# Performance work log

Hardware: AMD Instinct MI355X
Metric: run time of the kernel (lower is better)

Reference implementation:

```python
import jax, jax.numpy as jnp
import numpy as np

B, T, D, H = 4, 2048, 1024, 16
HD = D // H  # head_dim = 64


def _make_freqs():
    # standard RoPE angles: theta_i = 10000^{-2i/hd}
    inv_freq = 1.0 / (10000.0 ** (np.arange(0, HD, 2, dtype=np.float32) / HD))  # [HD/2]
    angles = np.arange(T, dtype=np.float32)[:, None] * inv_freq[None, :]        # [T, HD/2]
    return jnp.asarray(np.cos(angles)), jnp.asarray(np.sin(angles))


def setup_inputs() -> dict:
    key = jax.random.key(0)
    ks = jax.random.split(key, 5)
    freqs_cos, freqs_sin = _make_freqs()
    s = 1.0 / np.sqrt(D)
    return {
        "q": jax.random.normal(ks[0], (B, T, D), jnp.float32),
        "freqs_cos": freqs_cos,
        "freqs_sin": freqs_sin,
        "qkv_w": jax.random.normal(ks[1], (3 * D, D), jnp.float32) * s,
        "qkv_b": jax.random.normal(ks[2], (3 * D,), jnp.float32) * 0.01,
        "o_w": jax.random.normal(ks[3], (D, D), jnp.float32) * s,
        "o_b": jax.random.normal(ks[4], (D,), jnp.float32) * 0.01,
    }


def _apply_rope(x, cos, sin):
    # x: [B, T, H, HD]; cos/sin: [T, HD/2]
    xr = x.reshape(*x.shape[:-1], HD // 2, 2)
    x0, x1 = xr[..., 0], xr[..., 1]
    c = cos[None, :, None, :]
    s = sin[None, :, None, :]
    o0 = x0 * c - x1 * s
    o1 = x0 * s + x1 * c
    return jnp.stack([o0, o1], axis=-1).reshape(x.shape)


def reference(q, freqs_cos, freqs_sin, qkv_w, qkv_b, o_w, o_b):
    # fused QKV projection (torch Linear: x @ W.T + b)
    qkv = q @ qkv_w.T + qkv_b                      # [B, T, 3D]
    qh, kh, vh = jnp.split(qkv, 3, axis=-1)
    qh = qh.reshape(B, T, H, HD)
    kh = kh.reshape(B, T, H, HD)
    vh = vh.reshape(B, T, H, HD)
    qh = _apply_rope(qh, freqs_cos, freqs_sin)
    kh = _apply_rope(kh, freqs_cos, freqs_sin)
    # scaled dot-product attention, no mask, no dropout (eval)
    scale = 1.0 / np.sqrt(HD)
    scores = jnp.einsum('bqhd,bkhd->bhqk', qh, kh) * scale
    probs = jax.nn.softmax(scores, axis=-1)
    out = jnp.einsum('bhqk,bkhd->bqhd', probs, vh).reshape(B, T, D)
    return out @ o_w.T + o_b
```

## Files before the change

kernel.cpp:

```cpp
#include <hip/hip_runtime.h>

#define B_  4
#define T_  2048
#define D_  1024
#define H_  16
#define HD_ 64
#define M_  8192
#define N1_ 3072
#define K_  1024

typedef __bf16 bf16x8 __attribute__((ext_vector_type(8)));
typedef float  f32x4  __attribute__((ext_vector_type(4)));
typedef float  f32x16 __attribute__((ext_vector_type(16)));

__device__ __forceinline__ unsigned short f2bf(float f) {
  union { float f; unsigned u; } v; v.f = f;
  unsigned u = v.u;
  unsigned r = (u + 0x7fffu + ((u >> 16) & 1u)) >> 16;
  return (unsigned short)r;
}
__device__ __forceinline__ float bf2f(unsigned short h) {
  union { unsigned u; float f; } v; v.u = ((unsigned)h) << 16;
  return v.f;
}
__device__ __forceinline__ unsigned pk2(float a, float b) {
  union { __bf16 h[2]; unsigned u; } t;
  t.h[0] = (__bf16)a; t.h[1] = (__bf16)b;
  return t.u;
}
__device__ __forceinline__ void plswap(unsigned &a, unsigned &b) {
  asm("v_permlane32_swap_b32 %0, %1" : "+v"(a), "+v"(b));
}
__device__ __forceinline__ float fexp2(float x) {
  float r;
  asm("v_exp_f32 %0, %1" : "=v"(r) : "v"(x));
  return r;
}

__device__ __forceinline__ void gl_lds16(const unsigned short* g, unsigned short* l) {
  __builtin_amdgcn_global_load_lds(
      (const __attribute__((address_space(1))) unsigned int*)g,
      (__attribute__((address_space(3))) unsigned int*)l,
      16, 0, 0);
}

#define NQ4  ((M_*K_)/4)
#define NW14 ((N1_*K_)/4)
#define NW24 ((D_*K_)/4)
__global__ void cvt_all(const float* __restrict__ q, const float* __restrict__ w1,
                        const float* __restrict__ w2,
                        unsigned short* __restrict__ qo, unsigned short* __restrict__ w1o,
                        unsigned short* __restrict__ w2o) {
  int i = blockIdx.x * 256 + threadIdx.x;
  const float* in; unsigned short* out; int idx;
  if (i < NQ4)              { in = q;  out = qo;  idx = i; }
  else if (i < NQ4 + NW14)  { in = w1; out = w1o; idx = i - NQ4; }
  else if (i < NQ4 + NW14 + NW24) { in = w2; out = w2o; idx = i - NQ4 - NW14; }
  else return;
  float4 f = ((const float4*)in)[idx];
  ushort4 o;
  o.x = f2bf(f.x); o.y = f2bf(f.y); o.z = f2bf(f.z); o.w = f2bf(f.w);
  ((ushort4*)out)[idx] = o;
}

__global__ __launch_bounds__(256) void gemm_qkv(
    const unsigned short* __restrict__ A,
    const unsigned short* __restrict__ W,
    const float* __restrict__ bias,
    unsigned short* __restrict__ Qg,
    unsigned short* __restrict__ Kg,
    unsigned short* __restrict__ Vt,
    const float* __restrict__ cosb, const float* __restrict__ sinb)
{
  __shared__ unsigned short As[128*64];
  __shared__ unsigned short Bs[128*64];
  const int tid = threadIdx.x;
  const int lane = tid & 63, wave = tid >> 6;
  const int wr = wave >> 1, wc = wave & 1;
  const int lr = lane & 15, lg = lane >> 4;
  const int sw = lr & 7;
  const long m0 = (long)blockIdx.x * 128;
  const int  n0 = blockIdx.y * 128;

  f32x4 acc[4][4];
#pragma unroll
  for (int i = 0; i < 4; ++i)
#pragma unroll
    for (int j = 0; j < 4; ++j) acc[i][j] = (f32x4){0.f,0.f,0.f,0.f};

  for (int kt = 0; kt < K_/64; ++kt) {
    __syncthreads();
#pragma unroll
    for (int p = 0; p < 4; ++p) {
      int slot = p*256 + tid;
      int row = slot >> 3, sc = slot & 7, ch = sc ^ (row & 7);
      gl_lds16(A + (m0 + row)*K_ + kt*64 + ch*8, &As[slot*8]);
      gl_lds16(W + ((long)n0 + row)*K_ + kt*64 + ch*8, &Bs[slot*8]);
    }
    __syncthreads();
#pragma unroll
    for (int kk = 0; kk < 2; ++kk) {
      bf16x8 af[4], bfr[4];
#pragma unroll
      for (int i = 0; i < 4; ++i) {
        af[i]  = *(const bf16x8*)&As[(wr*64 + i*16 + lr)*64 + (((lg + 4*kk) ^ sw) * 8)];
        bfr[i] = *(const bf16x8*)&Bs[(wc*64 + i*16 + lr)*64 + (((lg + 4*kk) ^ sw) * 8)];
      }
#pragma unroll
      for (int i = 0; i < 4; ++i)
#pragma unroll
        for (int j = 0; j < 4; ++j)
          acc[i][j] = __builtin_amdgcn_mfma_f32_16x16x32_bf16(af[i], bfr[j], acc[i][j], 0, 0, 0);
    }
  }

#pragma unroll
  for (int j = 0; j < 4; ++j) {
    int n = n0 + wc*64 + j*16 + lr;
    float bv = bias[n];
    int part = n >> 10;
    int d = n & 1023;
    int h = d >> 6, hd = d & 63;
    if (part == 2) {
#pragma unroll
      for (int i = 0; i < 4; ++i) {
        long m = m0 + wr*64 + i*16 + lg*4;
        int b = (int)(m >> 11), t = (int)(m & 2047);
        ushort4 st;
        st.x = f2bf(acc[i][j][0] + bv);
        st.y = f2bf(acc[i][j][1] + bv);
        st.z = f2bf(acc[i][j][2] + bv);
        st.w = f2bf(acc[i][j][3] + bv);
        *(ushort4*)(Vt + ((long)((b*H_ + h)*HD_ + hd))*T_ + t) = st;
      }
    } else if (part == 0) {
#pragma unroll
      for (int i = 0; i < 4; ++i) {
#pragma unroll
        for (int r = 0; r < 4; ++r) {
          long m = m0 + wr*64 + i*16 + lg*4 + r;
          int b = (int)(m >> 11), t = (int)(m & 2047);
          Qg[(((long)(b*H_ + h))*T_ + t)*HD_ + hd] = f2bf(acc[i][j][r] + bv);
        }
      }
    } else {
      const int u   = hd >> 1;
      const int odd = lr & 1;
#pragma unroll
      for (int i = 0; i < 4; ++i) {
#pragma unroll
        for (int r = 0; r < 4; ++r) {
          long m = m0 + wr*64 + i*16 + lg*4 + r;
          int b = (int)(m >> 11), t = (int)(m & 2047);
          float v = acc[i][j][r] + bv;
          float p = __shfl_xor(v, 1);
          float cu = cosb[t*32 + u], su = sinb[t*32 + u];
          float res = odd ? (p*su + v*cu) : (v*cu - p*su);
          Kg[(((long)(b*H_ + h))*T_ + t)*HD_ + hd] = f2bf(res);
        }
      }
    }
  }
}

__global__ __launch_bounds__(256) void flash_attn(
    const unsigned short* __restrict__ Qg, const unsigned short* __restrict__ Kg,
    const unsigned short* __restrict__ Vt, unsigned short* __restrict__ attn,
    const float* __restrict__ cosb, const float* __restrict__ sinb)
{
  __shared__ unsigned short Ks0[64*64], Vs0[64*64];
  __shared__ unsigned short Ks1[64*64], Vs1[64*64];
  const int tid = threadIdx.x, lane = tid & 63, wave = tid >> 6;
  const int lq = lane & 31, hi = lane >> 5;
  const int id = blockIdx.x;
  const int bh = (id & 7)*8 + ((id >> 3) & 7);
  const int q0 = (id >> 6)*128 + wave*32;
  const long kvbase = (long)bh * T_ * HD_;
  const int fsw = (lq & 7) ^ (lq >> 3);

  bf16x8 qf[4];
  {
    const int tq = q0 + lq;
    const unsigned short* qrow = Qg + kvbase + (long)tq*HD_;
    const float* crow = cosb + tq*32;
    const float* srow = sinb + tq*32;
    const float scl = 0.125f * 1.44269504f;
#pragma unroll
    for (int c = 0; c < 4; ++c) {
      bf16x8 raw = *(const bf16x8*)(qrow + c*16 + hi*8);
      const unsigned short* e = (const unsigned short*)&raw;
      bf16x8 outv;
#pragma unroll
      for (int j = 0; j < 4; ++j) {
        float x0 = bf2f(e[2*j]), x1 = bf2f(e[2*j+1]);
        float cv = crow[c*8 + hi*4 + j], sv = srow[c*8 + hi*4 + j];
        outv[2*j]   = (__bf16)((x0*cv - x1*sv) * scl);
        outv[2*j+1] = (__bf16)((x0*sv + x1*cv) * scl);
      }
      qf[c] = outv;
    }
  }

  bf16x8 onesv;
#pragma unroll
  for (int r = 0; r < 8; ++r) onesv[r] = (__bf16)1.0f;

  f32x16 oA, oB;
  f32x16 lacc;
#pragma unroll
  for (int r = 0; r < 16; ++r) { oA[r] = 0.f; oB[r] = 0.f; lacc[r] = 0.f; }

  const int slotA = tid, slotB = 256 + tid;
  const int rwA = slotA >> 3, rwB = slotB >> 3;
  const int chA = (slotA & 7) ^ ((rwA & 7) ^ ((rwA >> 3) & 7));
  const int chB = (slotB & 7) ^ ((rwB & 7) ^ ((rwB >> 3) & 7));
  const unsigned short* KsrcA = Kg + kvbase + (long)rwA*HD_ + chA*8;
  const unsigned short* KsrcB = Kg + kvbase + (long)rwB*HD_ + chB*8;
  const unsigned short* VsrcA = Vt + (long)(bh*HD_ + rwA)*T_ + chA*8;
  const unsigned short* VsrcB = Vt + (long)(bh*HD_ + rwB)*T_ + chB*8;

#define STAGE0(kt) {                                      \
    gl_lds16(KsrcA + (kt)*64*HD_, &Ks0[slotA*8]);         \
    gl_lds16(KsrcB + (kt)*64*HD_, &Ks0[slotB*8]);         \
    gl_lds16(VsrcA + (kt)*64,     &Vs0[slotA*8]);         \
    gl_lds16(VsrcB + (kt)*64,     &Vs0[slotB*8]);         \
  }
#define STAGE1(kt) {                                      \
    gl_lds16(KsrcA + (kt)*64*HD_, &Ks1[slotA*8]);         \
    gl_lds16(KsrcB + (kt)*64*HD_, &Ks1[slotB*8]);         \
    gl_lds16(VsrcA + (kt)*64,     &Vs1[slotA*8]);         \
    gl_lds16(VsrcB + (kt)*64,     &Vs1[slotB*8]);         \
  }

#define FBODY(KSB, VSB)                                                                   \
  _Pragma("unroll")                                                                       \
  for (int kf = 0; kf < 2; ++kf) {                                                        \
    bf16x8 ka[4];                                                                         \
    _Pragma("unroll")                                                                     \
    for (int c = 0; c < 4; ++c)                                                           \
      ka[c] = *(const bf16x8*)&KSB[(kf*32 + lq)*64 + (((2*c + hi) ^ fsw ^ (kf*4)) * 8)];  \
    f32x16 cf;                                                                            \
    _Pragma("unroll")                                                                     \
    for (int r = 0; r < 16; ++r) cf[r] = 0.f;                                             \
    __builtin_amdgcn_s_setprio(1);                                                        \
    cf = __builtin_amdgcn_mfma_f32_32x32x16_bf16(ka[0], qf[0], cf, 0, 0, 0);              \
    cf = __builtin_amdgcn_mfma_f32_32x32x16_bf16(ka[1], qf[1], cf, 0, 0, 0);              \
    cf = __builtin_amdgcn_mfma_f32_32x32x16_bf16(ka[2], qf[2], cf, 0, 0, 0);              \
    cf = __builtin_amdgcn_mfma_f32_32x32x16_bf16(ka[3], qf[3], cf, 0, 0, 0);              \
    __builtin_amdgcn_s_setprio(0);                                                        \
    float p[16];                                                                          \
    _Pragma("unroll")                                                                     \
    for (int r = 0; r < 16; ++r) p[r] = fexp2(cf[r]);                                     \
    unsigned qx0 = pk2(p[0],  p[1]),  qy0 = pk2(p[2],  p[3]);                             \
    unsigned qx1 = pk2(p[4],  p[5]),  qy1 = pk2(p[6],  p[7]);                             \
    unsigned qx2 = pk2(p[8],  p[9]),  qy2 = pk2(p[10], p[11]);                            \
    unsigned qx3 = pk2(p[12], p[13]), qy3 = pk2(p[14], p[15]);                            \
    plswap(qx0, qx1); plswap(qy0, qy1);                                                   \
    plswap(qx2, qx3); plswap(qy2, qy3);                                                   \
    union { unsigned w[4]; bf16x8 v; } u0, u1;                                            \
    u0.w[0] = qx0; u0.w[1] = qy0; u0.w[2] = qx1; u0.w[3] = qy1;                           \
    u1.w[0] = qx2; u1.w[1] = qy2; u1.w[2] = qx3; u1.w[3] = qy3;                           \
    bf16x8 pf0 = u0.v, pf1 = u1.v;                                                        \
    bf16x8 va00 = *(const bf16x8*)&VSB[(lq)*64      + (((4*kf + 0 + hi) ^ fsw) * 8)];     \
    bf16x8 va01 = *(const bf16x8*)&VSB[(lq)*64      + (((4*kf + 2 + hi) ^ fsw) * 8)];     \
    bf16x8 va10 = *(const bf16x8*)&VSB[(32 + lq)*64 + (((4*kf + 0 + hi) ^ fsw ^ 4) * 8)]; \
    bf16x8 va11 = *(const bf16x8*)&VSB[(32 + lq)*64 + (((4*kf + 2 + hi) ^ fsw ^ 4) * 8)]; \
    __builtin_amdgcn_s_setprio(1);                                                        \
    oA = __builtin_amdgcn_mfma_f32_32x32x16_bf16(va00, pf0, oA, 0, 0, 0);                 \
    oA = __builtin_amdgcn_mfma_f32_32x32x16_bf16(va01, pf1, oA, 0, 0, 0);                 \
    oB = __builtin_amdgcn_mfma_f32_32x32x16_bf16(va10, pf0, oB, 0, 0, 0);                 \
    oB = __builtin_amdgcn_mfma_f32_32x32x16_bf16(va11, pf1, oB, 0, 0, 0);                 \
    lacc = __builtin_amdgcn_mfma_f32_32x32x16_bf16(onesv, pf0, lacc, 0, 0, 0);            \
    lacc = __builtin_amdgcn_mfma_f32_32x32x16_bf16(onesv, pf1, lacc, 0, 0, 0);            \
    __builtin_amdgcn_s_setprio(0);                                                        \
  }

  STAGE0(0);
  __syncthreads();

  for (int kt = 0; kt < T_/64; kt += 2) {
    STAGE1(kt + 1);
    FBODY(Ks0, Vs0);
    __syncthreads();
    if (kt + 2 < T_/64) STAGE0(kt + 2);
    FBODY(Ks1, Vs1);
    __syncthreads();
  }
#undef STAGE0
#undef STAGE1
#undef FBODY

  float l = lacc[0];
  int b = bh >> 4, h = bh & 15;
  float inv = 1.0f / l;
  long rowb = ((long)(b*T_ + q0 + lq))*D_ + h*HD_;
#pragma unroll
  for (int g = 0; g < 4; ++g) {
    ushort4 st;
    st.x = f2bf(oA[4*g+0] * inv);
    st.y = f2bf(oA[4*g+1] * inv);
    st.z = f2bf(oA[4*g+2] * inv);
    st.w = f2bf(oA[4*g+3] * inv);
    *(ushort4*)(attn + rowb + 8*g + 4*hi) = st;
  }
#pragma unroll
  for (int g = 0; g < 4; ++g) {
    ushort4 st;
    st.x = f2bf(oB[4*g+0] * inv);
    st.y = f2bf(oB[4*g+1] * inv);
    st.z = f2bf(oB[4*g+2] * inv);
    st.w = f2bf(oB[4*g+3] * inv);
    *(ushort4*)(attn + rowb + 32 + 8*g + 4*hi) = st;
  }
}

__global__ __launch_bounds__(256) void gemm_out(
    const unsigned short* __restrict__ A,
    const unsigned short* __restrict__ W,
    const float* __restrict__ bias,
    float* __restrict__ C)
{
  __shared__ unsigned short As[128*64];
  __shared__ unsigned short Bs[128*64];
  const int tid = threadIdx.x;
  const int lane = tid & 63, wave = tid >> 6;
  const int wr = wave >> 1, wc = wave & 1;
  const int lr = lane & 15, lg = lane >> 4;
  const int sw = lr & 7;
  const long m0 = (long)blockIdx.x * 128;
  const int  n0 = blockIdx.y * 128;

  f32x4 acc[4][4];
#pragma unroll
  for (int i = 0; i < 4; ++i)
#pragma unroll
    for (int j = 0; j < 4; ++j) acc[i][j] = (f32x4){0.f,0.f,0.f,0.f};

  for (int kt = 0; kt < K_/64; ++kt) {
    __syncthreads();
#pragma unroll
    for (int p = 0; p < 4; ++p) {
      int slot = p*256 + tid;
      int row = slot >> 3, sc = slot & 7, ch = sc ^ (row & 7);
      gl_lds16(A + (m0 + row)*K_ + kt*64 + ch*8, &As[slot*8]);
      gl_lds16(W + ((long)n0 + row)*K_ + kt*64 + ch*8, &Bs[slot*8]);
    }
    __syncthreads();
#pragma unroll
    for (int kk = 0; kk < 2; ++kk) {
      bf16x8 af[4], bfr[4];
#pragma unroll
      for (int i = 0; i < 4; ++i) {
        af[i]  = *(const bf16x8*)&As[(wr*64 + i*16 + lr)*64 + (((lg + 4*kk) ^ sw) * 8)];
        bfr[i] = *(const bf16x8*)&Bs[(wc*64 + i*16 + lr)*64 + (((lg + 4*kk) ^ sw) * 8)];
      }
#pragma unroll
      for (int i = 0; i < 4; ++i)
#pragma unroll
        for (int j = 0; j < 4; ++j)
          acc[i][j] = __builtin_amdgcn_mfma_f32_16x16x32_bf16(af[i], bfr[j], acc[i][j], 0, 0, 0);
    }
  }

#pragma unroll
  for (int j = 0; j < 4; ++j) {
    int n = n0 + wc*64 + j*16 + lr;
    float bv = bias[n];
#pragma unroll
    for (int i = 0; i < 4; ++i) {
#pragma unroll
      for (int r = 0; r < 4; ++r) {
        long m = m0 + wr*64 + i*16 + lg*4 + r;
        C[m*D_ + n] = acc[i][j][r] + bv;
      }
    }
  }
}

extern "C" void kernel_launch(void* const* d_in, const int* in_sizes, int n_in,
                              void* d_out, int out_size, void* d_ws, size_t ws_size,
                              hipStream_t stream)
{
  const float* q     = (const float*)d_in[0];
  const float* fcos  = (const float*)d_in[1];
  const float* fsin  = (const float*)d_in[2];
  const float* qkv_w = (const float*)d_in[3];
  const float* qkv_b = (const float*)d_in[4];
  const float* o_w   = (const float*)d_in[5];
  const float* o_b   = (const float*)d_in[6];
  float* out = (float*)d_out;

  char* ws = (char*)d_ws;
  unsigned short* qbf  = (unsigned short*)(ws);
  unsigned short* w1bf = (unsigned short*)(ws + 16777216);
  unsigned short* w2bf = (unsigned short*)(ws + 16777216 + 6291456);
  unsigned short* Qg   = (unsigned short*)(ws + 25165824);
  unsigned short* Kg   = (unsigned short*)(ws + 41943040);
  unsigned short* Vt   = (unsigned short*)(ws + 58720256);

  int ncvt = NQ4 + NW14 + NW24;
  cvt_all<<<(ncvt + 255)/256, 256, 0, stream>>>(q, qkv_w, o_w, qbf, w1bf, w2bf);

  dim3 g1(M_/128, N1_/128);
  gemm_qkv<<<g1, 256, 0, stream>>>(qbf, w1bf, qkv_b, Qg, Kg, Vt, fcos, fsin);

  unsigned short* attn = qbf;
  flash_attn<<<1024, 256, 0, stream>>>(Qg, Kg, Vt, attn, fcos, fsin);

  dim3 g2(M_/128, D_/128);
  gemm_out<<<g2, 256, 0, stream>>>(attn, w2bf, o_b, out);
}
```

Baseline: 206.5 us.

## Process two query tiles per wave in flash attention, sum row totals with VALU

Each wave now handles two 32-row query tiles, rows q0 and q0+128, and shares every K and V fragment loaded from LDS between them. That doubles the MFMA work per LDS read and halves the grid to 512 blocks. The row-sum MFMAs against a ones vector are replaced by scalar float adds of the exp values plus a cross-half shuffle. The kernel keeps the fixed no-max softmax shape, and the change raises register pressure and may lower occupancy and wave-level parallelism.

```diff
diff --git a/kernel.cpp b/kernel.cpp
--- a/kernel.cpp
+++ b/kernel.cpp
@@ -174,41 +174,41 @@
   const int lq = lane & 31, hi = lane >> 5;
   const int id = blockIdx.x;
   const int bh = (id & 7)*8 + ((id >> 3) & 7);
-  const int q0 = (id >> 6)*128 + wave*32;
+  const int q0 = (id >> 6)*256 + wave*32;
   const long kvbase = (long)bh * T_ * HD_;
   const int fsw = (lq & 7) ^ (lq >> 3);
 
-  bf16x8 qf[4];
+  bf16x8 qfA[4], qfB[4];
   {
-    const int tq = q0 + lq;
-    const unsigned short* qrow = Qg + kvbase + (long)tq*HD_;
-    const float* crow = cosb + tq*32;
-    const float* srow = sinb + tq*32;
     const float scl = 0.125f * 1.44269504f;
 #pragma unroll
-    for (int c = 0; c < 4; ++c) {
-      bf16x8 raw = *(const bf16x8*)(qrow + c*16 + hi*8);
-      const unsigned short* e = (const unsigned short*)&raw;
-      bf16x8 outv;
-#pragma unroll
-      for (int j = 0; j < 4; ++j) {
-        float x0 = bf2f(e[2*j]), x1 = bf2f(e[2*j+1]);
-        float cv = crow[c*8 + hi*4 + j], sv = srow[c*8 + hi*4 + j];
-        outv[2*j]   = (__bf16)((x0*cv - x1*sv) * scl);
-        outv[2*j+1] = (__bf16)((x0*sv + x1*cv) * scl);
-      }
-      qf[c] = outv;
-    }
-  }
-
-  bf16x8 onesv;
-#pragma unroll
-  for (int r = 0; r < 8; ++r) onesv[r] = (__bf16)1.0f;
+    for (int g = 0; g < 2; ++g) {
+      const int tq = q0 + g*128 + lq;
+      const unsigned short* qrow = Qg + kvbase + (long)tq*HD_;
+      const float* crow = cosb + tq*32;
+      const float* srow = sinb + tq*32;
+#pragma unroll
+      for (int c = 0; c < 4; ++c) {
+        bf16x8 raw = *(const bf16x8*)(qrow + c*16 + hi*8);
+        const unsigned short* e = (const unsigned short*)&raw;
+        bf16x8 outv;
+#pragma unroll
+        for (int j = 0; j < 4; ++j) {
+          float x0 = bf2f(e[2*j]), x1 = bf2f(e[2*j+1]);
+          float cv = crow[c*8 + hi*4 + j], sv = srow[c*8 + hi*4 + j];
+          outv[2*j]   = (__bf16)((x0*cv - x1*sv) * scl);
+          outv[2*j+1] = (__bf16)((x0*sv + x1*cv) * scl);
+        }
+        if (g == 0) qfA[c] = outv; else qfB[c] = outv;
+      }
+    }
+  }
 
   f32x16 oA, oB;
-  f32x16 lacc;
-#pragma unroll
-  for (int r = 0; r < 16; ++r) { oA[r] = 0.f; oB[r] = 0.f; lacc[r] = 0.f; }
+  f32x16 oC, oD;
+#pragma unroll
+  for (int r = 0; r < 16; ++r) { oA[r] = 0.f; oB[r] = 0.f; oC[r] = 0.f; oD[r] = 0.f; }
+  float lA = 0.f, lB = 0.f;
 
   const int slotA = tid, slotB = 256 + tid;
   const int rwA = slotA >> 3, rwB = slotB >> 3;
@@ -239,39 +239,65 @@
     _Pragma("unroll")                                                                     \
     for (int c = 0; c < 4; ++c)                                                           \
       ka[c] = *(const bf16x8*)&KSB[(kf*32 + lq)*64 + (((2*c + hi) ^ fsw ^ (kf*4)) * 8)];  \
-    f32x16 cf;                                                                            \
+    f32x16 cfA, cfB;                                                                      \
     _Pragma("unroll")                                                                     \
-    for (int r = 0; r < 16; ++r) cf[r] = 0.f;                                             \
+    for (int r = 0; r < 16; ++r) { cfA[r] = 0.f; cfB[r] = 0.f; }                          \
     __builtin_amdgcn_s_setprio(1);                                                        \
-    cf = __builtin_amdgcn_mfma_f32_32x32x16_bf16(ka[0], qf[0], cf, 0, 0, 0);              \
-    cf = __builtin_amdgcn_mfma_f32_32x32x16_bf16(ka[1], qf[1], cf, 0, 0, 0);              \
-    cf = __builtin_amdgcn_mfma_f32_32x32x16_bf16(ka[2], qf[2], cf, 0, 0, 0);              \
-    cf = __builtin_amdgcn_mfma_f32_32x32x16_bf16(ka[3], qf[3], cf, 0, 0, 0);              \
+    cfA = __builtin_amdgcn_mfma_f32_32x32x16_bf16(ka[0], qfA[0], cfA, 0, 0, 0);           \
+    cfB = __builtin_amdgcn_mfma_f32_32x32x16_bf16(ka[0], qfB[0], cfB, 0, 0, 0);           \
+    cfA = __builtin_amdgcn_mfma_f32_32x32x16_bf16(ka[1], qfA[1], cfA, 0, 0, 0);           \
+    cfB = __builtin_amdgcn_mfma_f32_32x32x16_bf16(ka[1], qfB[1], cfB, 0, 0, 0);           \
+    cfA = __builtin_amdgcn_mfma_f32_32x32x16_bf16(ka[2], qfA[2], cfA, 0, 0, 0);           \
+    cfB = __builtin_amdgcn_mfma_f32_32x32x16_bf16(ka[2], qfB[2], cfB, 0, 0, 0);           \
+    cfA = __builtin_amdgcn_mfma_f32_32x32x16_bf16(ka[3], qfA[3], cfA, 0, 0, 0);           \
+    cfB = __builtin_amdgcn_mfma_f32_32x32x16_bf16(ka[3], qfB[3], cfB, 0, 0, 0);           \
     __builtin_amdgcn_s_setprio(0);                                                        \
-    float p[16];                                                                          \
+    float p[16], p2[16];                                                                  \
     _Pragma("unroll")                                                                     \
-    for (int r = 0; r < 16; ++r) p[r] = fexp2(cf[r]);                                     \
-    unsigned qx0 = pk2(p[0],  p[1]),  qy0 = pk2(p[2],  p[3]);                             \
-    unsigned qx1 = pk2(p[4],  p[5]),  qy1 = pk2(p[6],  p[7]);                             \
-    unsigned qx2 = pk2(p[8],  p[9]),  qy2 = pk2(p[10], p[11]);                            \
-    unsigned qx3 = pk2(p[12], p[13]), qy3 = pk2(p[14], p[15]);                            \
-    plswap(qx0, qx1); plswap(qy0, qy1);                                                   \
-    plswap(qx2, qx3); plswap(qy2, qy3);                                                   \
-    union { unsigned w[4]; bf16x8 v; } u0, u1;                                            \
-    u0.w[0] = qx0; u0.w[1] = qy0; u0.w[2] = qx1; u0.w[3] = qy1;                           \
-    u1.w[0] = qx2; u1.w[1] = qy2; u1.w[2] = qx3; u1.w[3] = qy3;                           \
-    bf16x8 pf0 = u0.v, pf1 = u1.v;                                                        \
+    for (int r = 0; r < 16; ++r) { p[r] = fexp2(cfA[r]); p2[r] = fexp2(cfB[r]); }         \
+    {                                                                                     \
+      float a0 = (p[0]+p[1]) + (p[2]+p[3]);                                               \
+      float a1 = (p[4]+p[5]) + (p[6]+p[7]);                                               \
+      float a2 = (p[8]+p[9]) + (p[10]+p[11]);                                             \
+      float a3 = (p[12]+p[13]) + (p[14]+p[15]);                                           \
+      lA += (a0 + a1) + (a2 + a3);                                                        \
+      float b0 = (p2[0]+p2[1]) + (p2[2]+p2[3]);                                           \
+      float b1 = (p2[4]+p2[5]) + (p2[6]+p2[7]);                                           \
+      float b2 = (p2[8]+p2[9]) + (p2[10]+p2[11]);                                         \
+      float b3 = (p2[12]+p2[13]) + (p2[14]+p2[15]);                                       \
+      lB += (b0 + b1) + (b2 + b3);                                                        \
+    }                                                                                     \
+    unsigned ax0 = pk2(p[0],  p[1]),  ay0 = pk2(p[2],  p[3]);                             \
+    unsigned ax1 = pk2(p[4],  p[5]),  ay1 = pk2(p[6],  p[7]);                             \
+    unsigned ax2 = pk2(p[8],  p[9]),  ay2 = pk2(p[10], p[11]);                            \
+    unsigned ax3 = pk2(p[12], p[13]), ay3 = pk2(p[14], p[15]);                            \
+    plswap(ax0, ax1); plswap(ay0, ay1);                                                   \
+    plswap(ax2, ax3); plswap(ay2, ay3);                                                   \
+    unsigned bx0 = pk2(p2[0],  p2[1]),  by0 = pk2(p2[2],  p2[3]);                         \
+    unsigned bx1 = pk2(p2[4],  p2[5]),  by1 = pk2(p2[6],  p2[7]);                         \
+    unsigned bx2 = pk2(p2[8],  p2[9]),  by2 = pk2(p2[10], p2[11]);                        \
+    unsigned bx3 = pk2(p2[12], p2[13]), by3 = pk2(p2[14], p2[15]);                        \
+    plswap(bx0, bx1); plswap(by0, by1);                                                   \
+    plswap(bx2, bx3); plswap(by2, by3);                                                   \
+    union { unsigned w[4]; bf16x8 v; } uA0, uA1, uB0, uB1;                                \
+    uA0.w[0] = ax0; uA0.w[1] = ay0; uA0.w[2] = ax1; uA0.w[3] = ay1;                       \
+    uA1.w[0] = ax2; uA1.w[1] = ay2; uA1.w[2] = ax3; uA1.w[3] = ay3;                       \
+    uB0.w[0] = bx0; uB0.w[1] = by0; uB0.w[2] = bx1; uB0.w[3] = by1;                       \
+    uB1.w[0] = bx2; uB1.w[1] = by2; uB1.w[2] = bx3; uB1.w[3] = by3;                       \
+    bf16x8 pfA0 = uA0.v, pfA1 = uA1.v, pfB0 = uB0.v, pfB1 = uB1.v;                        \
     bf16x8 va00 = *(const bf16x8*)&VSB[(lq)*64      + (((4*kf + 0 + hi) ^ fsw) * 8)];     \
     bf16x8 va01 = *(const bf16x8*)&VSB[(lq)*64      + (((4*kf + 2 + hi) ^ fsw) * 8)];     \
     bf16x8 va10 = *(const bf16x8*)&VSB[(32 + lq)*64 + (((4*kf + 0 + hi) ^ fsw ^ 4) * 8)]; \
     bf16x8 va11 = *(const bf16x8*)&VSB[(32 + lq)*64 + (((4*kf + 2 + hi) ^ fsw ^ 4) * 8)]; \
     __builtin_amdgcn_s_setprio(1);                                                        \
-    oA = __builtin_amdgcn_mfma_f32_32x32x16_bf16(va00, pf0, oA, 0, 0, 0);                 \
-    oA = __builtin_amdgcn_mfma_f32_32x32x16_bf16(va01, pf1, oA, 0, 0, 0);                 \
-    oB = __builtin_amdgcn_mfma_f32_32x32x16_bf16(va10, pf0, oB, 0, 0, 0);                 \
-    oB = __builtin_amdgcn_mfma_f32_32x32x16_bf16(va11, pf1, oB, 0, 0, 0);                 \
-    lacc = __builtin_amdgcn_mfma_f32_32x32x16_bf16(onesv, pf0, lacc, 0, 0, 0);            \
-    lacc = __builtin_amdgcn_mfma_f32_32x32x16_bf16(onesv, pf1, lacc, 0, 0, 0);            \
+    oA = __builtin_amdgcn_mfma_f32_32x32x16_bf16(va00, pfA0, oA, 0, 0, 0);                \
+    oC = __builtin_amdgcn_mfma_f32_32x32x16_bf16(va00, pfB0, oC, 0, 0, 0);                \
+    oA = __builtin_amdgcn_mfma_f32_32x32x16_bf16(va01, pfA1, oA, 0, 0, 0);                \
+    oC = __builtin_amdgcn_mfma_f32_32x32x16_bf16(va01, pfB1, oC, 0, 0, 0);                \
+    oB = __builtin_amdgcn_mfma_f32_32x32x16_bf16(va10, pfA0, oB, 0, 0, 0);                \
+    oD = __builtin_amdgcn_mfma_f32_32x32x16_bf16(va10, pfB0, oD, 0, 0, 0);                \
+    oB = __builtin_amdgcn_mfma_f32_32x32x16_bf16(va11, pfA1, oB, 0, 0, 0);                \
+    oD = __builtin_amdgcn_mfma_f32_32x32x16_bf16(va11, pfB1, oD, 0, 0, 0);                \
     __builtin_amdgcn_s_setprio(0);                                                        \
   }
 
@@ -290,27 +316,48 @@
 #undef STAGE1
 #undef FBODY
 
-  float l = lacc[0];
+  lA += __shfl_xor(lA, 32);
+  lB += __shfl_xor(lB, 32);
   int b = bh >> 4, h = bh & 15;
-  float inv = 1.0f / l;
-  long rowb = ((long)(b*T_ + q0 + lq))*D_ + h*HD_;
+  float invA = 1.0f / lA;
+  float invB = 1.0f / lB;
+  long rowbA = ((long)(b*T_ + q0 + lq))*D_ + h*HD_;
+  long rowbB = ((long)(b*T_ + q0 + 128 + lq))*D_ + h*HD_;
 #pragma unroll
   for (int g = 0; g < 4; ++g) {
     ushort4 st;
-    st.x = f2bf(oA[4*g+0] * inv);
-    st.y = f2bf(oA[4*g+1] * inv);
-    st.z = f2bf(oA[4*g+2] * inv);
-    st.w = f2bf(oA[4*g+3] * inv);
-    *(ushort4*)(attn + rowb + 8*g + 4*hi) = st;
+    st.x = f2bf(oA[4*g+0] * invA);
+    st.y = f2bf(oA[4*g+1] * invA);
+    st.z = f2bf(oA[4*g+2] * invA);
+    st.w = f2bf(oA[4*g+3] * invA);
+    *(ushort4*)(attn + rowbA + 8*g + 4*hi) = st;
   }
 #pragma unroll
   for (int g = 0; g < 4; ++g) {
     ushort4 st;
-    st.x = f2bf(oB[4*g+0] * inv);
-    st.y = f2bf(oB[4*g+1] * inv);
-    st.z = f2bf(oB[4*g+2] * inv);
-    st.w = f2bf(oB[4*g+3] * inv);
-    *(ushort4*)(attn + rowb + 32 + 8*g + 4*hi) = st;
+    st.x = f2bf(oB[4*g+0] * invA);
+    st.y = f2bf(oB[4*g+1] * invA);
+    st.z = f2bf(oB[4*g+2] * invA);
+    st.w = f2bf(oB[4*g+3] * invA);
+    *(ushort4*)(attn + rowbA + 32 + 8*g + 4*hi) = st;
+  }
+#pragma unroll
+  for (int g = 0; g < 4; ++g) {
+    ushort4 st;
+    st.x = f2bf(oC[4*g+0] * invB);
+    st.y = f2bf(oC[4*g+1] * invB);
+    st.z = f2bf(oC[4*g+2] * invB);
+    st.w = f2bf(oC[4*g+3] * invB);
+    *(ushort4*)(attn + rowbB + 8*g + 4*hi) = st;
+  }
+#pragma unroll
+  for (int g = 0; g < 4; ++g) {
+    ushort4 st;
+    st.x = f2bf(oD[4*g+0] * invB);
+    st.y = f2bf(oD[4*g+1] * invB);
+    st.z = f2bf(oD[4*g+2] * invB);
+    st.w = f2bf(oD[4*g+3] * invB);
+    *(ushort4*)(attn + rowbB + 32 + 8*g + 4*hi) = st;
   }
 }
 
@@ -405,7 +452,7 @@
   gemm_qkv<<<g1, 256, 0, stream>>>(qbf, w1bf, qkv_b, Qg, Kg, Vt, fcos, fsin);
 
   unsigned short* attn = qbf;
-  flash_attn<<<1024, 256, 0, stream>>>(Qg, Kg, Vt, attn, fcos, fsin);
+  flash_attn<<<512, 256, 0, stream>>>(Qg, Kg, Vt, attn, fcos, fsin);
 
   dim3 g2(M_/128, D_/128);
   gemm_out<<<g2, 256, 0, stream>>>(attn, w2bf, o_b, out);
```

Result: slower. 212.6 us (+2.9%).
